# Kernel optimization log

Hardware: AMD Instinct MI355X
Metric: run time of the kernel (lower is better)

The kernel has to match this reference:

```python
import jax, jax.numpy as jnp
import numpy as np
from jax.scipy.special import logsumexp

TEMPERATURE = 0.1
BETA = 0.999
EPS = 1e-8
HARD_K = 10  # min(num_classes // 4, 10) with num_classes = 1000


def _l2norm(x, axis=-1):
    return x * jax.lax.rsqrt(jnp.sum(x * x, axis=axis, keepdims=True) + 1e-24)


def setup_inputs() -> dict:
    key = jax.random.key(0)
    k1, k2, k3, k4, k5 = jax.random.split(key, 5)
    B, D, C, M = 4096, 1024, 1000, 32768
    return {
        "image_features": jax.random.normal(k1, (B, D), dtype=jnp.float32),
        "prompts": jax.random.normal(k2, (C, D), dtype=jnp.float32),
        "labels": jax.random.randint(k3, (B, C), 0, 2, dtype=jnp.int32),
        "memory_features": jax.random.normal(k4, (M, D), dtype=jnp.float32),
        "memory_labels": jax.random.randint(k5, (M, C), 0, 2, dtype=jnp.int32),
        "mem_ptr": 16384,
    }


def reference(image_features, prompts, labels, memory_features, memory_labels, mem_ptr):
    B, D = image_features.shape
    C = prompts.shape[0]
    labels_f = labels.astype(jnp.float32)

    # z_img = F.normalize(image_features)
    z_img = _l2norm(image_features, axis=1)

    # class weights (effective-number reweighting), computed from this batch's labels
    counts = labels_f.sum(axis=0)                              # [C]
    effective_num = 1.0 - jnp.power(jnp.float32(BETA), counts)
    weights = (1.0 - BETA) / (effective_num + EPS)
    weights = weights / jnp.sum(weights) * C                   # [C]

    # memory bank update (detached write of current batch at ptr), then use [:ptr+B]
    mem_f = memory_features.at[mem_ptr:mem_ptr + B].set(jax.lax.stop_gradient(z_img))
    mem_l = memory_labels.at[mem_ptr:mem_ptr + B].set(labels)
    used = mem_ptr + B  # static

    enhanced_features = jnp.concatenate([z_img, mem_f[:used]], axis=0)     # [N, D]
    enhanced_labels = jnp.concatenate([labels_f, mem_l[:used].astype(jnp.float32)], axis=0)  # [N, C]

    z_prompts = _l2norm(prompts, axis=1)                       # [C, D]
    sim = (enhanced_features @ z_prompts.T) / TEMPERATURE      # [N, C]

    pos_mask = enhanced_labels > 0                             # [N, C]

    # hard negatives: top-K similarities among negatives define the keep threshold
    sim_for_neg = jnp.where(pos_mask, -jnp.inf, sim)
    hard_neg_vals, _ = jax.lax.top_k(sim_for_neg, HARD_K)      # [N, K]
    min_hard_neg = hard_neg_vals[:, -1:]                       # [N, 1]
    neg_mask = (~pos_mask) & (sim >= min_hard_neg)
    full_mask = pos_mask | neg_mask

    lse = logsumexp(jnp.where(full_mask, sim, -jnp.inf), axis=1)  # [N]
    log_prob = sim - lse[:, None]                              # [N, C]

    posf = pos_mask.astype(sim.dtype)
    pos_w = posf * weights[None, :]                            # [N, C]
    weight_sums = pos_w.sum(axis=1)                            # [N]
    loss_num = (pos_w * (-log_prob)).sum(axis=1)               # [N]

    valid = weight_sums > 0
    loss_per_sample = jnp.where(valid, loss_num / (weight_sums + EPS), 0.0)
    n_valid = jnp.maximum(valid.sum(), 1)
    attr_loss = loss_per_sample.sum() / n_valid.astype(sim.dtype)
    # single attribute -> total_loss / num_valid_attrs == attr_loss
    return attr_loss
```

## Files before the change

kernel.cpp:

```cpp
#include <hip/hip_runtime.h>
#include <math.h>

#define BN    4096
#define DD    1024
#define CC    1000
#define MM    32768
#define ROWS_CAP 32768
#define SIMLD 1024


typedef __attribute__((ext_vector_type(8))) int   int8v;
typedef __attribute__((ext_vector_type(16))) float f32x16;

__device__ __forceinline__ float wave_max_f(float v) {
#pragma unroll
  for (int off = 32; off >= 1; off >>= 1) v = fmaxf(v, __shfl_xor(v, off, 64));
  return v;
}
__device__ __forceinline__ float wave_sum_f(float v) {
#pragma unroll
  for (int off = 32; off >= 1; off >>= 1) v += __shfl_xor(v, off, 64);
  return v;
}

__device__ __forceinline__ short f2bf(float f) {
  union { float f; unsigned u; } v; v.f = f;
  unsigned r = v.u + 0x7FFF + ((v.u >> 16) & 1);
  return (short)(r >> 16);
}
__device__ __forceinline__ float bf2f(unsigned short u) {
  union { unsigned u; float f; } v; v.u = ((unsigned)u) << 16;
  return v.f;
}

__device__ __forceinline__ int pack4(float a, float b, float c, float d) {
  int p = __builtin_amdgcn_cvt_pk_fp8_f32(a, b, 0, false);
  p = __builtin_amdgcn_cvt_pk_fp8_f32(c, d, p, true);
  return p;
}

__device__ __forceinline__ void gload16(const unsigned char* g, unsigned char* l) {
  __builtin_amdgcn_global_load_lds(
      (const __attribute__((address_space(1))) unsigned int*)g,
      (__attribute__((address_space(3))) unsigned int*)l, 16, 0, 0);
}

__global__ __launch_bounds__(256) void count_kernel(const int* __restrict__ labels,
                                                    int* __restrict__ counts) {
  const int c = blockIdx.x * 256 + threadIdx.x;
  if (c >= CC) return;
  const int b0 = blockIdx.y * 32;
  int s = 0;
#pragma unroll
  for (int b = 0; b < 32; ++b) s += labels[(size_t)(b0 + b) * CC + c];
  atomicAdd(&counts[c], s);
}

__global__ __launch_bounds__(1024) void weights_kernel(const int* __restrict__ counts,
                                                       float* __restrict__ weights) {
  const int t = threadIdx.x;
  float w = 0.f;
  if (t < CC) {
    float cnt = (float)counts[t];
    float en = 1.0f - expf(cnt * logf(0.999f));
    w = (1.0f - 0.999f) / (en + 1e-8f);
  }
  float s = wave_sum_f(w);
  __shared__ float part[16];
  if ((t & 63) == 0) part[t >> 6] = s;
  __syncthreads();
  float tot = 0.f;
#pragma unroll
  for (int i = 0; i < 16; ++i) tot += part[i];
  if (t < CC) weights[t] = w * ((float)CC / tot);
}

__global__ __launch_bounds__(256) void conv_kernel(const float* __restrict__ img,
                                                   const float* __restrict__ prompts,
                                                   const float* __restrict__ mem,
                                                   const int* __restrict__ memptr,
                                                   unsigned char* __restrict__ A,
                                                   unsigned char* __restrict__ B) {
  const int t = threadIdx.x;
  const int lane = t & 63;
  const int gr = blockIdx.x * 4 + (t >> 6);

  const float* src = nullptr;
  unsigned char* dst;
  float extraScale = 1.0f;
  bool needNorm = false;

  if (gr >= ROWS_CAP) {
    const int row = gr - ROWS_CAP;
    dst = B + (size_t)(row >> 7) * 131072 + (size_t)(row & 127) * 16;
    if (row < CC) {
      src = prompts + (size_t)row * DD;
      needNorm = true;
      extraScale = 10.0f;
    }
  } else {
    const int nrows = BN + memptr[0];
    const int padded = (nrows + 127) & ~127;
    if (gr >= padded) return;
    dst = A + (size_t)(gr >> 7) * 131072 + (size_t)(gr & 127) * 16;
    if (gr < nrows) {
      if (gr < BN) { src = img + (size_t)gr * DD; needNorm = true; }
      else         { src = mem + (size_t)(gr - BN) * DD; }
    }
  }

  int4 o = {0, 0, 0, 0};
  if (src) {
    const float4* s4 = (const float4*)src + lane * 4;
    float4 a = s4[0], b = s4[1], c = s4[2], d = s4[3];
    float sc = extraScale;
    if (needNorm) {
      float ss = a.x * a.x + a.y * a.y + a.z * a.z + a.w * a.w
               + b.x * b.x + b.y * b.y + b.z * b.z + b.w * b.w
               + c.x * c.x + c.y * c.y + c.z * c.z + c.w * c.w
               + d.x * d.x + d.y * d.y + d.z * d.z + d.w * d.w;
      ss = wave_sum_f(ss);
      sc = extraScale * rsqrtf(ss + 1e-24f);
    }
    o.x = pack4(a.x * sc, a.y * sc, a.z * sc, a.w * sc);
    o.y = pack4(b.x * sc, b.y * sc, b.z * sc, b.w * sc);
    o.z = pack4(c.x * sc, c.y * sc, c.z * sc, c.w * sc);
    o.w = pack4(d.x * sc, d.y * sc, d.z * sc, d.w * sc);
  }
  *(int4*)(dst + (size_t)lane * 2048) = o;
}

__global__ __launch_bounds__(256) void gemm_mx(const unsigned char* __restrict__ A,
                                               const unsigned char* __restrict__ Bm,
                                               const int* __restrict__ memptr,
                                               short* __restrict__ simbf, int lo) {
  const int f = blockIdx.x;
  const int x = f & 7;
  const int s = f >> 3;
  const int c = s & 7;
  const int rt = (s >> 3) * 8 + x;

  const int nrows = BN + memptr[0];
  const int row0 = rt * 128;
  if (lo + row0 >= nrows) return;
  const int c0 = c * 128;

  __shared__ unsigned char As[16384];
  __shared__ unsigned char Bs[16384];

  const int t = threadIdx.x;
  const int lane = t & 63;
  const int wid = t >> 6;
  const int wm = (wid >> 1) * 64;
  const int wn = (wid & 1) * 64;

  const unsigned char* gaT = A + (size_t)(lo + row0) * DD;
  const unsigned char* gbT = Bm + (size_t)c0 * DD;
  unsigned char* lA = As + t * 16;
  unsigned char* lB = Bs + t * 16;

  f32x16 acc[2][2] = {};
  const int q = lane >> 5;
  const int rr = lane & 31;

  for (int k0 = 0; k0 < DD; k0 += 128) {
    const size_t kb = (size_t)k0 * 128;
#pragma unroll
    for (int p = 0; p < 4; ++p)
      gload16(gaT + kb + p * 4096 + t * 16, lA + p * 4096);
#pragma unroll
    for (int p = 0; p < 4; ++p)
      gload16(gbT + kb + p * 4096 + t * 16, lB + p * 4096);
    __syncthreads();
#pragma unroll
    for (int h = 0; h < 2; ++h) {
      int8v af[2], bfv[2];
      const int kc = h * 4 + q * 2;
#pragma unroll
      for (int mi = 0; mi < 2; ++mi) {
        const unsigned char* pa = As + kc * 2048 + (wm + mi * 32 + rr) * 16;
        int4 lo4 = *(const int4*)pa;
        int4 hi4 = *(const int4*)(pa + 2048);
        af[mi][0] = lo4.x; af[mi][1] = lo4.y; af[mi][2] = lo4.z; af[mi][3] = lo4.w;
        af[mi][4] = hi4.x; af[mi][5] = hi4.y; af[mi][6] = hi4.z; af[mi][7] = hi4.w;
      }
#pragma unroll
      for (int ni = 0; ni < 2; ++ni) {
        const unsigned char* pb = Bs + kc * 2048 + (wn + ni * 32 + rr) * 16;
        int4 lo4 = *(const int4*)pb;
        int4 hi4 = *(const int4*)(pb + 2048);
        bfv[ni][0] = lo4.x; bfv[ni][1] = lo4.y; bfv[ni][2] = lo4.z; bfv[ni][3] = lo4.w;
        bfv[ni][4] = hi4.x; bfv[ni][5] = hi4.y; bfv[ni][6] = hi4.z; bfv[ni][7] = hi4.w;
      }
#pragma unroll
      for (int mi = 0; mi < 2; ++mi)
#pragma unroll
        for (int ni = 0; ni < 2; ++ni)
          acc[mi][ni] = __builtin_amdgcn_mfma_scale_f32_32x32x64_f8f6f4(
              af[mi], bfv[ni], acc[mi][ni], 0, 0, 0, 127, 0, 127);
    }
    __syncthreads();
  }

  const int cl = lane & 31;
  const int r4 = 4 * (lane >> 5);
#pragma unroll
  for (int mi = 0; mi < 2; ++mi)
#pragma unroll
    for (int ni = 0; ni < 2; ++ni) {
      f32x16 v = acc[mi][ni];
      const int colg = c0 + wn + ni * 32 + cl;
      const int rbase = row0 + wm + mi * 32 + r4;
#pragma unroll
      for (int reg = 0; reg < 16; ++reg) {
        const int rowl = rbase + (reg & 3) + 8 * (reg >> 2);
        simbf[(size_t)rowl * SIMLD + colg] = f2bf(v[reg]);
      }
    }
}

__global__ __launch_bounds__(256) void rowpost_kernel(
    const short* __restrict__ simbf, const int* __restrict__ labels,
    const int* __restrict__ mlabels, const float* __restrict__ weights,
    const int* __restrict__ memptr, float* __restrict__ lps_arr,
    float* __restrict__ valid_arr, int chunk_lo) {
  __shared__ float wlds[1024];
  {
    const int t = threadIdx.x;
#pragma unroll
    for (int i = 0; i < 4; ++i) {
      int c = t + i * 256;
      wlds[c] = (c < CC) ? weights[c] : 0.f;
    }
  }
  __syncthreads();

  const int nrows = BN + memptr[0];
  const int wid = threadIdx.x >> 6;
  const int lane = threadIdx.x & 63;
  const int row = chunk_lo + blockIdx.x * 4 + wid;
  if (row >= ROWS_CAP) return;
  if (row >= nrows) {
    if (lane == 0) { lps_arr[row] = 0.f; valid_arr[row] = 0.f; }
    return;
  }

  const unsigned short* srow = (const unsigned short*)simbf + (size_t)(row - chunk_lo) * SIMLD;
  const int* lrow = (row < BN) ? labels + (size_t)row * CC
                               : mlabels + (size_t)(row - BN) * CC;
  const int cbase = lane * 16;

  unsigned short sraw[16];
  *(ulonglong2*)&sraw[0] = *(const ulonglong2*)(srow + cbase);
  *(ulonglong2*)&sraw[8] = *(const ulonglong2*)(srow + cbase + 8);
  int lab[16];
#pragma unroll
  for (int g = 0; g < 4; ++g) {
    int c = cbase + g * 4;
    if (c + 3 < CC) {
      *(int4*)&lab[g * 4] = *(const int4*)(lrow + c);
    } else {
#pragma unroll
      for (int u = 0; u < 4; ++u) lab[g * 4 + u] = (c + u < CC) ? lrow[c + u] : 0;
    }
  }

  float sv[16];
  bool pv[16];
  float vneg[16];
#pragma unroll
  for (int j = 0; j < 16; ++j) {
    int c = cbase + j;
    bool ok = (c < CC);
    float sf = bf2f(sraw[j]);
    bool p = ok && (lab[j] > 0);
    sv[j] = ok ? sf : -INFINITY;
    pv[j] = p;
    vneg[j] = (ok && !p) ? sf : -INFINITY;
  }

  float v10 = -INFINITY;
  for (int r = 0; r < 10; ++r) {
    float lmx = -INFINITY;
#pragma unroll
    for (int j = 0; j < 16; ++j) lmx = fmaxf(lmx, vneg[j]);
    lmx = wave_max_f(lmx);
#pragma unroll
    for (int j = 0; j < 16; ++j) if (vneg[j] == lmx) vneg[j] = -INFINITY;
    v10 = lmx;
  }

  float mmax = -INFINITY;
#pragma unroll
  for (int j = 0; j < 16; ++j) {
    if (pv[j] || sv[j] >= v10) mmax = fmaxf(mmax, sv[j]);
  }
  mmax = wave_max_f(mmax);

  float esum = 0.f, wsum = 0.f, wsim = 0.f;
#pragma unroll
  for (int j = 0; j < 16; ++j) {
    int c = cbase + j;
    if (c < CC) {
      if (pv[j] || sv[j] >= v10) esum += expf(sv[j] - mmax);
      if (pv[j]) { float w = wlds[c]; wsum += w; wsim += w * sv[j]; }
    }
  }
  esum = wave_sum_f(esum);
  wsum = wave_sum_f(wsum);
  wsim = wave_sum_f(wsim);

  if (lane == 0) {
    float lse = mmax + logf(esum);
    bool valid = (wsum > 0.f);
    float lps = valid ? (wsum * lse - wsim) / (wsum + 1e-8f) : 0.f;
    float mult = (row < BN) ? 2.f : 1.f;
    lps_arr[row] = mult * lps;
    valid_arr[row] = valid ? mult : 0.f;
  }
}

__global__ __launch_bounds__(1024) void reduce_kernel(const float* __restrict__ lps_arr,
                                                      const float* __restrict__ valid_arr,
                                                      float* __restrict__ out) {
  const int t = threadIdx.x;
  const float4* l4 = (const float4*)lps_arr;
  const float4* v4 = (const float4*)valid_arr;
  float s1 = 0.f, s2 = 0.f;
#pragma unroll
  for (int i = 0; i < 8; ++i) {
    float4 a = l4[t + i * 1024];
    float4 b = v4[t + i * 1024];
    s1 += a.x + a.y + a.z + a.w;
    s2 += b.x + b.y + b.z + b.w;
  }
  s1 = wave_sum_f(s1);
  s2 = wave_sum_f(s2);
  __shared__ float p1[16], p2[16];
  if ((t & 63) == 0) { p1[t >> 6] = s1; p2[t >> 6] = s2; }
  __syncthreads();
  if (t == 0) {
    float a = 0.f, b = 0.f;
#pragma unroll
    for (int i = 0; i < 16; ++i) { a += p1[i]; b += p2[i]; }
    out[0] = a / fmaxf(b, 1.0f);
  }
}

extern "C" void kernel_launch(void* const* d_in, const int* in_sizes, int n_in,
                              void* d_out, int out_size, void* d_ws, size_t ws_size,
                              hipStream_t stream) {
  const float* img     = (const float*)d_in[0];
  const float* prompts = (const float*)d_in[1];
  const int*   labels  = (const int*)d_in[2];
  const float* mem     = (const float*)d_in[3];
  const int*   mlabels = (const int*)d_in[4];
  const int*   memptr  = (const int*)d_in[5];
  float* out = (float*)d_out;
  char* ws = (char*)d_ws;

  int*   counts  = (int*)(ws + 0);
  float* weights = (float*)(ws + 4096);
  float* lps_arr = (float*)(ws + 8192);
  float* val_arr = (float*)(ws + 139264);
  unsigned char* Bf8 = (unsigned char*)(ws + 270336);
  unsigned char* Af8 = (unsigned char*)(ws + 1318912);
  const size_t fixed = 1318912 + (size_t)ROWS_CAP * DD;
  short* simbf = (short*)(ws + fixed);

  long long avail = (long long)ws_size - (long long)fixed;
  int chunk = (int)(avail / (SIMLD * 2));
  chunk &= ~1023;
  if (chunk < 1024) chunk = 1024;
  if (chunk > ROWS_CAP) chunk = ROWS_CAP;

  hipMemsetAsync(ws, 0, 4096, stream);

  conv_kernel<<<(ROWS_CAP + 1024) / 4, 256, 0, stream>>>(img, prompts, mem, memptr, Af8, Bf8);
  count_kernel<<<dim3((CC + 255) / 256, BN / 32), 256, 0, stream>>>(labels, counts);
  weights_kernel<<<1, 1024, 0, stream>>>(counts, weights);

  for (int lo = 0; lo < ROWS_CAP; lo += chunk) {
    int rows = (ROWS_CAP - lo < chunk) ? (ROWS_CAP - lo) : chunk;
    int rowTiles = rows / 128;
    gemm_mx<<<8 * rowTiles, 256, 0, stream>>>(Af8, Bf8, memptr, simbf, lo);
    rowpost_kernel<<<rows / 4, 256, 0, stream>>>(simbf, labels, mlabels, weights, memptr,
                                                 lps_arr, val_arr, lo);
  }
  reduce_kernel<<<1, 1024, 0, stream>>>(lps_arr, val_arr, out);
}
```

Baseline: 342.4 us.

## Fuse label counting into conversion kernel, stage fp8 tiles via LDS, inline weights

Label counting moves into extra blocks of the conversion kernel, and the class-weight computation is recomputed per block inside rowpost. This removes two kernel launches, count_kernel and weights_kernel. The conversion kernel now handles 64 rows per block: each row is normalised and packed to fp8, written into a swizzled 64KB LDS tile, then stored to the tiled A/B layout as coalesced 16-byte chunks instead of the previous strided scattered stores. The cost is heavier LDS use, which limits occupancy in the conversion kernel, plus redundant exp/log work in every rowpost block.

```diff
diff --git a/kernel.cpp b/kernel.cpp
--- a/kernel.cpp
+++ b/kernel.cpp
@@ -9,6 +9,10 @@
 #define SIMLD 1024
 
 
+#define NGROUP_A 512
+#define NGROUP_B 16
+#define NCOUNT   512
+
 typedef __attribute__((ext_vector_type(8))) int   int8v;
 typedef __attribute__((ext_vector_type(16))) float f32x16;
 
@@ -43,36 +47,6 @@
   __builtin_amdgcn_global_load_lds(
       (const __attribute__((address_space(1))) unsigned int*)g,
       (__attribute__((address_space(3))) unsigned int*)l, 16, 0, 0);
-}
-
-__global__ __launch_bounds__(256) void count_kernel(const int* __restrict__ labels,
-                                                    int* __restrict__ counts) {
-  const int c = blockIdx.x * 256 + threadIdx.x;
-  if (c >= CC) return;
-  const int b0 = blockIdx.y * 32;
-  int s = 0;
-#pragma unroll
-  for (int b = 0; b < 32; ++b) s += labels[(size_t)(b0 + b) * CC + c];
-  atomicAdd(&counts[c], s);
-}
-
-__global__ __launch_bounds__(1024) void weights_kernel(const int* __restrict__ counts,
-                                                       float* __restrict__ weights) {
-  const int t = threadIdx.x;
-  float w = 0.f;
-  if (t < CC) {
-    float cnt = (float)counts[t];
-    float en = 1.0f - expf(cnt * logf(0.999f));
-    w = (1.0f - 0.999f) / (en + 1e-8f);
-  }
-  float s = wave_sum_f(w);
-  __shared__ float part[16];
-  if ((t & 63) == 0) part[t >> 6] = s;
-  __syncthreads();
-  float tot = 0.f;
-#pragma unroll
-  for (int i = 0; i < 16; ++i) tot += part[i];
-  if (t < CC) weights[t] = w * ((float)CC / tot);
 }
 
 __global__ __launch_bounds__(256) void conv_kernel(const float* __restrict__ img,
@@ -80,54 +54,80 @@
                                                    const float* __restrict__ mem,
                                                    const int* __restrict__ memptr,
                                                    unsigned char* __restrict__ A,
-                                                   unsigned char* __restrict__ B) {
+                                                   unsigned char* __restrict__ B,
+                                                   const int* __restrict__ labels,
+                                                   int* __restrict__ counts) {
+  const int blk = blockIdx.x;
+
+  if (blk >= NGROUP_A + NGROUP_B) {
+    const int ci = blk - (NGROUP_A + NGROUP_B);
+    const int c = (ci & 3) * 256 + threadIdx.x;
+    if (c >= CC) return;
+    const int b0 = (ci >> 2) * 32;
+    int s = 0;
+#pragma unroll
+    for (int b = 0; b < 32; ++b) s += labels[(size_t)(b0 + b) * CC + c];
+    atomicAdd(&counts[c], s);
+    return;
+  }
+
+  __shared__ unsigned char tile[65536];
   const int t = threadIdx.x;
   const int lane = t & 63;
-  const int gr = blockIdx.x * 4 + (t >> 6);
-
-  const float* src = nullptr;
-  unsigned char* dst;
-  float extraScale = 1.0f;
-  bool needNorm = false;
-
-  if (gr >= ROWS_CAP) {
-    const int row = gr - ROWS_CAP;
-    dst = B + (size_t)(row >> 7) * 131072 + (size_t)(row & 127) * 16;
-    if (row < CC) {
-      src = prompts + (size_t)row * DD;
-      needNorm = true;
-      extraScale = 10.0f;
-    }
-  } else {
-    const int nrows = BN + memptr[0];
-    const int padded = (nrows + 127) & ~127;
-    if (gr >= padded) return;
-    dst = A + (size_t)(gr >> 7) * 131072 + (size_t)(gr & 127) * 16;
-    if (gr < nrows) {
-      if (gr < BN) { src = img + (size_t)gr * DD; needNorm = true; }
-      else         { src = mem + (size_t)(gr - BN) * DD; }
-    }
-  }
-
-  int4 o = {0, 0, 0, 0};
-  if (src) {
-    const float4* s4 = (const float4*)src + lane * 4;
-    float4 a = s4[0], b = s4[1], c = s4[2], d = s4[3];
-    float sc = extraScale;
-    if (needNorm) {
-      float ss = a.x * a.x + a.y * a.y + a.z * a.z + a.w * a.w
-               + b.x * b.x + b.y * b.y + b.z * b.z + b.w * b.w
-               + c.x * c.x + c.y * c.y + c.z * c.z + c.w * c.w
-               + d.x * d.x + d.y * d.y + d.z * d.z + d.w * d.w;
-      ss = wave_sum_f(ss);
-      sc = extraScale * rsqrtf(ss + 1e-24f);
-    }
-    o.x = pack4(a.x * sc, a.y * sc, a.z * sc, a.w * sc);
-    o.y = pack4(b.x * sc, b.y * sc, b.z * sc, b.w * sc);
-    o.z = pack4(c.x * sc, c.y * sc, c.z * sc, c.w * sc);
-    o.w = pack4(d.x * sc, d.y * sc, d.z * sc, d.w * sc);
-  }
-  *(int4*)(dst + (size_t)lane * 2048) = o;
+  const int wid = t >> 6;
+  const int nrows = BN + memptr[0];
+  const int padded = (nrows + 127) & ~127;
+
+  const bool isB = (blk >= NGROUP_A);
+  const int g = isB ? (blk - NGROUP_A) : blk;
+  const int rowBase = g * 64;
+  if (!isB && rowBase >= padded) return;
+
+  unsigned char* dstBase = (isB ? B : A)
+      + (size_t)(rowBase >> 7) * 131072 + (size_t)(rowBase & 64) * 16;
+
+  for (int i = 0; i < 16; ++i) {
+    const int r = wid * 16 + i;
+    const int row = rowBase + r;
+    const float* src = nullptr;
+    float esc = 1.0f;
+    bool needNorm = false;
+    if (isB) {
+      if (row < CC) { src = prompts + (size_t)row * DD; needNorm = true; esc = 10.0f; }
+    } else {
+      if (row < BN)         { src = img + (size_t)row * DD; needNorm = true; }
+      else if (row < nrows) { src = mem + (size_t)(row - BN) * DD; }
+    }
+    int4 o = {0, 0, 0, 0};
+    if (src) {
+      const float4* s4 = (const float4*)src + lane * 4;
+      float4 a = s4[0], b = s4[1], c = s4[2], d = s4[3];
+      float sc = esc;
+      if (needNorm) {
+        float ss = a.x * a.x + a.y * a.y + a.z * a.z + a.w * a.w
+                 + b.x * b.x + b.y * b.y + b.z * b.z + b.w * b.w
+                 + c.x * c.x + c.y * c.y + c.z * c.z + c.w * c.w
+                 + d.x * d.x + d.y * d.y + d.z * d.z + d.w * d.w;
+        ss = wave_sum_f(ss);
+        sc = esc * rsqrtf(ss + 1e-24f);
+      }
+      o.x = pack4(a.x * sc, a.y * sc, a.z * sc, a.w * sc);
+      o.y = pack4(b.x * sc, b.y * sc, b.z * sc, b.w * sc);
+      o.z = pack4(c.x * sc, c.y * sc, c.z * sc, c.w * sc);
+      o.w = pack4(d.x * sc, d.y * sc, d.z * sc, d.w * sc);
+    }
+    *(int4*)(tile + lane * 1024 + (((r + lane) & 63) << 4)) = o;
+  }
+  __syncthreads();
+
+#pragma unroll
+  for (int p = 0; p < 16; ++p) {
+    const int ochunk = p * 256 + t;
+    const int kc = ochunk >> 6;
+    const int rl = ochunk & 63;
+    int4 v = *(const int4*)(tile + kc * 1024 + (((rl + kc) & 63) << 4));
+    *(int4*)(dstBase + (size_t)kc * 2048 + rl * 16) = v;
+  }
 }
 
 __global__ __launch_bounds__(256) void gemm_mx(const unsigned char* __restrict__ A,
@@ -221,19 +221,36 @@
 
 __global__ __launch_bounds__(256) void rowpost_kernel(
     const short* __restrict__ simbf, const int* __restrict__ labels,
-    const int* __restrict__ mlabels, const float* __restrict__ weights,
+    const int* __restrict__ mlabels, const int* __restrict__ counts,
     const int* __restrict__ memptr, float* __restrict__ lps_arr,
     float* __restrict__ valid_arr, int chunk_lo) {
   __shared__ float wlds[1024];
+  __shared__ float wpart[4];
   {
     const int t = threadIdx.x;
+    float wv[4];
+    float acc = 0.f;
 #pragma unroll
     for (int i = 0; i < 4; ++i) {
       int c = t + i * 256;
-      wlds[c] = (c < CC) ? weights[c] : 0.f;
-    }
-  }
-  __syncthreads();
+      float w = 0.f;
+      if (c < CC) {
+        float cnt = (float)counts[c];
+        float en = 1.0f - expf(cnt * logf(0.999f));
+        w = (1.0f - 0.999f) / (en + 1e-8f);
+      }
+      wv[i] = w;
+      acc += w;
+    }
+    float s = wave_sum_f(acc);
+    if ((t & 63) == 0) wpart[t >> 6] = s;
+    __syncthreads();
+    float tot = wpart[0] + wpart[1] + wpart[2] + wpart[3];
+    float sc = (float)CC / tot;
+#pragma unroll
+    for (int i = 0; i < 4; ++i) wlds[t + i * 256] = wv[i] * sc;
+    __syncthreads();
+  }
 
   const int nrows = BN + memptr[0];
   const int wid = threadIdx.x >> 6;
@@ -360,7 +377,6 @@
   char* ws = (char*)d_ws;
 
   int*   counts  = (int*)(ws + 0);
-  float* weights = (float*)(ws + 4096);
   float* lps_arr = (float*)(ws + 8192);
   float* val_arr = (float*)(ws + 139264);
   unsigned char* Bf8 = (unsigned char*)(ws + 270336);
@@ -376,15 +392,14 @@
 
   hipMemsetAsync(ws, 0, 4096, stream);
 
-  conv_kernel<<<(ROWS_CAP + 1024) / 4, 256, 0, stream>>>(img, prompts, mem, memptr, Af8, Bf8);
-  count_kernel<<<dim3((CC + 255) / 256, BN / 32), 256, 0, stream>>>(labels, counts);
-  weights_kernel<<<1, 1024, 0, stream>>>(counts, weights);
+  conv_kernel<<<NGROUP_A + NGROUP_B + NCOUNT, 256, 0, stream>>>(
+      img, prompts, mem, memptr, Af8, Bf8, labels, counts);
 
   for (int lo = 0; lo < ROWS_CAP; lo += chunk) {
     int rows = (ROWS_CAP - lo < chunk) ? (ROWS_CAP - lo) : chunk;
     int rowTiles = rows / 128;
     gemm_mx<<<8 * rowTiles, 256, 0, stream>>>(Af8, Bf8, memptr, simbf, lo);
-    rowpost_kernel<<<rows / 4, 256, 0, stream>>>(simbf, labels, mlabels, weights, memptr,
+    rowpost_kernel<<<rows / 4, 256, 0, stream>>>(simbf, labels, mlabels, counts, memptr,
                                                  lps_arr, val_arr, lo);
   }
   reduce_kernel<<<1, 1024, 0, stream>>>(lps_arr, val_arr, out);
```

After: 331.6 us. 3.1% less time.
